# Kernel optimization log

Hardware: AMD Instinct MI355X
Metric: run time of the kernel (lower is better)

## Reference

```python
import jax, jax.numpy as jnp
import numpy as np

LN_EPS = 1e-5
BN_EPS = 1e-5
ALPHA = 0.1

def _layer_norm(x):
    # F.layer_norm over last dim, no affine
    mu = jnp.mean(x, axis=-1, keepdims=True)
    var = jnp.var(x, axis=-1, keepdims=True)
    return (x - mu) * jax.lax.rsqrt(var + LN_EPS)

def setup_inputs() -> dict:
    key = jax.random.key(0)
    ks = jax.random.split(key, 12)
    N, Nh, D, Dq = 8192, 8192, 64, 64
    s = 1.0 / np.sqrt(D)
    inp = {
        "X": jax.random.normal(ks[0], (N, D), jnp.float32),
        "H": jax.random.normal(ks[1], (Nh, D), jnp.float32),
        "M": jax.random.uniform(ks[2], (N, Nh), jnp.float32),
        # Linear params (torch nn.Linear: y = x @ W.T + b), uniform init scale
        "Qw": jax.random.uniform(ks[3], (Dq, D), jnp.float32, -s, s),
        "Qb": jax.random.uniform(ks[4], (Dq,), jnp.float32, -s, s),
        "Kw": jax.random.uniform(ks[5], (Dq, D), jnp.float32, -s, s),
        "Kb": jax.random.uniform(ks[6], (Dq,), jnp.float32, -s, s),
        "Vw": jax.random.uniform(ks[7], (64, D), jnp.float32, -s, s),
        "Vb": jax.random.uniform(ks[8], (64,), jnp.float32, -s, s),
        # BatchNorm1d(64) eval-mode params
        "bn_gamma": jnp.ones((64,), jnp.float32),
        "bn_beta": jnp.zeros((64,), jnp.float32),
        "bn_mean": 0.1 * jax.random.normal(ks[9], (64,), jnp.float32),
        "bn_var": jax.random.uniform(ks[10], (64,), jnp.float32, 0.5, 1.5),
    }
    return inp

def reference(X, H, M, Qw, Qb, Kw, Kb, Vw, Vb, bn_gamma, bn_beta, bn_mean, bn_var):
    # K/Q branches: Linear + LayerNorm
    K = _layer_norm(H @ Kw.T + Kb)            # [Nh, Dq]
    Q = _layer_norm(X @ Qw.T + Qb)            # [N, Dq]
    # V branch: Linear + BatchNorm1d (eval mode; dropout is identity in eval)
    V = (H @ Vw.T + Vb - bn_mean) * jax.lax.rsqrt(bn_var + BN_EPS) * bn_gamma + bn_beta  # [Nh, 64]
    # Masked attention, softmax over dim=0 (columns)
    A = (Q @ K.T) * 0.125                     # [N, Nh]
    A = jax.nn.softmax(M * A, axis=0)
    # globel=True branch
    return ALPHA * (A @ V) + M @ H            # [N, 64]
```

## Files before the change

kernel.cpp:

```cpp
#include <hip/hip_runtime.h>
#include <hip/hip_bf16.h>
#include <math.h>

#define NN 8192
#define QSCALE (0.125f * 1.44269504088896f)
#define OSZ (8192*64)
#define NSL 16

typedef __attribute__((ext_vector_type(8))) short short8;
typedef __attribute__((ext_vector_type(16))) float f32x16;
typedef __attribute__((ext_vector_type(4))) float f32x4;

union W4 { unsigned u[4]; short8 v; };

__device__ inline unsigned short f2bf(float x) {
  union { float f; unsigned u; } t; t.f = x;
  unsigned r = t.u + 0x7fffu + ((t.u >> 16) & 1u);
  return (unsigned short)(r >> 16);
}
__device__ inline unsigned cvtpk(float lo, float hi) {
  unsigned r;
  asm("v_cvt_pk_bf16_f32 %0, %1, %2" : "=v"(r) : "v"(lo), "v"(hi));
  return r;
}
__device__ inline float fexp2(float x) {
  float r;
  asm("v_exp_f32 %0, %1" : "=v"(r) : "v"(x));
  return r;
}
__device__ inline void gload16(const float* g, float* l) {
  __builtin_amdgcn_global_load_lds(
      (const __attribute__((address_space(1))) void*)g,
      (__attribute__((address_space(3))) void*)l, 16, 0, 0);
}

__global__ __launch_bounds__(256) void qkv_kernel(
    const float* __restrict__ X, const float* __restrict__ H,
    const float* __restrict__ Qw, const float* __restrict__ Qb,
    const float* __restrict__ Kw, const float* __restrict__ Kb,
    const float* __restrict__ Vw, const float* __restrict__ Vb,
    const float* __restrict__ bng, const float* __restrict__ bnb,
    const float* __restrict__ bnm, const float* __restrict__ bnv,
    unsigned short* __restrict__ QP, unsigned short* __restrict__ KP,
    unsigned short* __restrict__ VP, unsigned short* __restrict__ HP)
{
  int wid = (blockIdx.x * blockDim.x + threadIdx.x) >> 6;
  int d = threadIdx.x & 63;
  float4 w[16];

  for (int fq = 0; fq < 16; fq++) w[fq] = *(const float4*)(Qw + d*64 + fq*4);
  for (int rr = 0; rr < 4; rr++) {
    int r = wid*4 + rr;
    float a = Qb[d];
    for (int fq = 0; fq < 16; fq++) {
      float4 xv = *(const float4*)(X + r*64 + fq*4);
      a += w[fq].x*xv.x + w[fq].y*xv.y + w[fq].z*xv.z + w[fq].w*xv.w;
    }
    float s = a;
    for (int off = 32; off; off >>= 1) s += __shfl_xor(s, off);
    float mean = s * (1.f/64.f);
    float c = a - mean;
    float s2 = c*c;
    for (int off = 32; off; off >>= 1) s2 += __shfl_xor(s2, off);
    float q = c * rsqrtf(s2*(1.f/64.f) + 1e-5f);
    QP[(d>>3)*65536 + r*8 + (d&7)] = f2bf(q * QSCALE);
  }
  for (int fq = 0; fq < 16; fq++) w[fq] = *(const float4*)(Kw + d*64 + fq*4);
  for (int rr = 0; rr < 4; rr++) {
    int r = wid*4 + rr;
    float a = Kb[d];
    for (int fq = 0; fq < 16; fq++) {
      float4 hv = *(const float4*)(H + r*64 + fq*4);
      a += w[fq].x*hv.x + w[fq].y*hv.y + w[fq].z*hv.z + w[fq].w*hv.w;
    }
    float s = a;
    for (int off = 32; off; off >>= 1) s += __shfl_xor(s, off);
    float mean = s * (1.f/64.f);
    float c = a - mean;
    float s2 = c*c;
    for (int off = 32; off; off >>= 1) s2 += __shfl_xor(s2, off);
    float k = c * rsqrtf(s2*(1.f/64.f) + 1e-5f);
    KP[(d>>3)*65536 + r*8 + (d&7)] = f2bf(k);
  }
  for (int fq = 0; fq < 16; fq++) w[fq] = *(const float4*)(Vw + d*64 + fq*4);
  float bscale = rsqrtf(bnv[d] + 1e-5f) * bng[d];
  for (int rr = 0; rr < 4; rr++) {
    int r = wid*4 + rr;
    float a = Vb[d];
    for (int fq = 0; fq < 16; fq++) {
      float4 hv = *(const float4*)(H + r*64 + fq*4);
      a += w[fq].x*hv.x + w[fq].y*hv.y + w[fq].z*hv.z + w[fq].w*hv.w;
    }
    float v = (a - bnm[d]) * bscale + bnb[d];
    VP[(r>>3)*512 + d*8 + (r&7)] = f2bf(v);
    HP[(r>>3)*512 + d*8 + (r&7)] = f2bf(H[r*64 + d]);
  }
}

__global__ __launch_bounds__(256) void pass1_kernel(
    const float* __restrict__ M, const unsigned short* __restrict__ QP,
    const unsigned short* __restrict__ KP, float* __restrict__ pd)
{
  int tid = threadIdx.x;
  int wj = (blockIdx.x * blockDim.x + tid) >> 6;
  int lane = tid & 63;
  int l31 = lane & 31, h = lane >> 5;
  int jb = wj & 255, slice = wj >> 8;
  int j = jb*32 + l31;

  short8 kb[4];
  for (int m = 0; m < 4; m++)
    kb[m] = *(const short8*)(KP + (2*m + h)*65536 + j*8);

  float Mv[16];
  {
    int i0 = slice*8*32;
#pragma unroll
    for (int r = 0; r < 16; r++) {
      int ir = (r&3) + 8*(r>>2) + 4*h;
      Mv[r] = M[(size_t)(i0 + ir)*NN + j];
    }
  }

  float d0 = 0.f, d1 = 0.f, d2 = 0.f, d3 = 0.f;
  for (int t = 0; t < 8; t++) {
    int i0 = (slice*8 + t) * 32;
    float Mn[16];
    if (t < 7) {
      int i1 = i0 + 32;
#pragma unroll
      for (int r = 0; r < 16; r++) {
        int ir = (r&3) + 8*(r>>2) + 4*h;
        Mn[r] = M[(size_t)(i1 + ir)*NN + j];
      }
    }

    f32x16 acc;
    for (int r = 0; r < 16; r++) acc[r] = 0.f;
    for (int m = 0; m < 4; m++) {
      short8 qa = *(const short8*)(QP + (2*m + h)*65536 + (size_t)(i0 + l31)*8);
      acc = __builtin_amdgcn_mfma_f32_32x32x16_bf16(qa, kb[m], acc, 0, 0, 0);
    }

    d0 += fexp2(acc[0]*Mv[0]) + fexp2(acc[4]*Mv[4]) + fexp2(acc[8]*Mv[8])   + fexp2(acc[12]*Mv[12]);
    d1 += fexp2(acc[1]*Mv[1]) + fexp2(acc[5]*Mv[5]) + fexp2(acc[9]*Mv[9])   + fexp2(acc[13]*Mv[13]);
    d2 += fexp2(acc[2]*Mv[2]) + fexp2(acc[6]*Mv[6]) + fexp2(acc[10]*Mv[10]) + fexp2(acc[14]*Mv[14]);
    d3 += fexp2(acc[3]*Mv[3]) + fexp2(acc[7]*Mv[7]) + fexp2(acc[11]*Mv[11]) + fexp2(acc[15]*Mv[15]);

    if (t < 7) {
#pragma unroll
      for (int r = 0; r < 16; r++) Mv[r] = Mn[r];
    }
  }
  float drun = (d0 + d1) + (d2 + d3);
  drun += __shfl_xor(drun, 32);
  if (lane < 32) pd[(size_t)slice*NN + j] = drun;
}

__global__ __launch_bounds__(256) void cv_kernel(
    const float* __restrict__ pd, const unsigned short* __restrict__ VP,
    unsigned short* __restrict__ VP2)
{
  __shared__ float cls[256];
  int tid = threadIdx.x;
  int j = blockIdx.x * 256 + tid;
  float Dv = 0.f;
  for (int s = 0; s < 32; s++) Dv += pd[(size_t)s*NN + j];
  cls[tid] = 0.1f / Dv;
  __syncthreads();

  int base = blockIdx.x * 2048;
#pragma unroll
  for (int k = 0; k < 8; k++) {
    int idx = base + k*256 + tid;
    int lj8 = (k*256 + tid) >> 6;
    const unsigned short* src = VP + (size_t)idx*8;
    unsigned short sv[8];
    *(short8*)sv = *(const short8*)src;
    float f[8];
#pragma unroll
    for (int e = 0; e < 8; e++)
      f[e] = __uint_as_float(((unsigned)sv[e]) << 16) * cls[lj8*8 + e];
    W4 o;
    o.u[0] = cvtpk(f[0], f[1]); o.u[1] = cvtpk(f[2], f[3]);
    o.u[2] = cvtpk(f[4], f[5]); o.u[3] = cvtpk(f[6], f[7]);
    *(short8*)(VP2 + (size_t)idx*8) = o.v;
  }
}

__global__ __launch_bounds__(256) void pass2_kernel(
    const float* __restrict__ M, const unsigned short* __restrict__ QP,
    const unsigned short* __restrict__ KP, const unsigned short* __restrict__ VP2,
    const unsigned short* __restrict__ HP, float* __restrict__ opart)
{
  __shared__ __align__(16) float tile[3][64*32];

  int iblk = blockIdx.x >> 4, slice = blockIdx.x & 15;
  int i0 = iblk * 64;
  int tid = threadIdx.x;
  int lane = tid & 63, wv = tid >> 6;
  int l31 = lane & 31, h = lane >> 5;
  int iq = wv & 1, dh = wv >> 1;
  int i_g = i0 + iq*32 + l31;
  int row = iq*32 + l31;
  int r7 = row & 7;

  short8 qb[4];
#pragma unroll
  for (int m = 0; m < 4; m++)
    qb[m] = *(const short8*)(QP + (2*m + h)*65536 + (size_t)i_g*8);

  int rsub = lane >> 3;
  int gdst = lane & 7;
  int c0base = slice*512;

#pragma unroll
  for (int t0 = 0; t0 < 2; t0++) {
    int c0 = c0base + t0*32;
#pragma unroll
    for (int k = 0; k < 2; k++) {
      int rloc = wv*16 + k*8 + rsub;
      int gs = gdst ^ (rloc & 7);
      gload16(M + (size_t)(i0 + rloc)*NN + c0 + gs*4,
              &tile[t0][(wv*16 + k*8)*32]);
    }
  }
  asm volatile("s_waitcnt vmcnt(2)" ::: "memory");
  __builtin_amdgcn_s_barrier();
  __builtin_amdgcn_sched_barrier(0);

  f32x16 oaccV, oaccH;
  for (int r = 0; r < 16; r++) { oaccV[r] = 0.f; oaccH[r] = 0.f; }

  for (int tm = 0; tm < 16; tm++) {
    int jt = slice*512 + tm*32;
    const float* mb = tile[tm % 3];

    short8 kb[4];
#pragma unroll
    for (int m = 0; m < 4; m++)
      kb[m] = *(const short8*)(KP + (2*m + h)*65536 + (size_t)(jt + l31)*8);
    int j8 = jt >> 3;
    const unsigned short* vbase = VP2 + (size_t)j8*512 + (dh*32 + l31)*8;
    const unsigned short* hbase = HP  + (size_t)j8*512 + (dh*32 + l31)*8;
    short8 vb1 = *(const short8*)(vbase + h*512);
    short8 vb2 = *(const short8*)(vbase + (2 + h)*512);
    short8 hb1 = *(const short8*)(hbase + h*512);
    short8 hb2 = *(const short8*)(hbase + (2 + h)*512);

    if (tm < 14) {
      int c0 = c0base + (tm+2)*32;
      float* dst = tile[(tm+2) % 3];
#pragma unroll
      for (int k = 0; k < 2; k++) {
        int rloc = wv*16 + k*8 + rsub;
        int gs = gdst ^ (rloc & 7);
        gload16(M + (size_t)(i0 + rloc)*NN + c0 + gs*4,
                &dst[(wv*16 + k*8)*32]);
      }
    }

    f32x4 mv[4];
#pragma unroll
    for (int q = 0; q < 4; q++) {
      int gr = 2*q + h;
      mv[q] = *(const f32x4*)&mb[row*32 + ((gr ^ r7) << 2)];
    }

    f32x16 saccA, saccB;
    for (int r = 0; r < 16; r++) { saccA[r] = 0.f; saccB[r] = 0.f; }
    saccA = __builtin_amdgcn_mfma_f32_32x32x16_bf16(kb[0], qb[0], saccA, 0, 0, 0);
    saccB = __builtin_amdgcn_mfma_f32_32x32x16_bf16(kb[2], qb[2], saccB, 0, 0, 0);
    saccA = __builtin_amdgcn_mfma_f32_32x32x16_bf16(kb[1], qb[1], saccA, 0, 0, 0);
    saccB = __builtin_amdgcn_mfma_f32_32x32x16_bf16(kb[3], qb[3], saccB, 0, 0, 0);

    float p[16];
#pragma unroll
    for (int q = 0; q < 4; q++) {
      p[4*q+0] = fexp2((saccA[4*q+0] + saccB[4*q+0]) * mv[q][0]);
      p[4*q+1] = fexp2((saccA[4*q+1] + saccB[4*q+1]) * mv[q][1]);
      p[4*q+2] = fexp2((saccA[4*q+2] + saccB[4*q+2]) * mv[q][2]);
      p[4*q+3] = fexp2((saccA[4*q+3] + saccB[4*q+3]) * mv[q][3]);
    }
    unsigned pu[8], mw[8];
#pragma unroll
    for (int k = 0; k < 8; k++) pu[k] = cvtpk(p[2*k], p[2*k+1]);
#pragma unroll
    for (int q = 0; q < 4; q++) {
      mw[2*q]   = cvtpk(mv[q][0], mv[q][1]);
      mw[2*q+1] = cvtpk(mv[q][2], mv[q][3]);
    }

    asm volatile("v_permlane32_swap_b32 %0, %1" : "+v"(pu[0]), "+v"(pu[2]));
    asm volatile("v_permlane32_swap_b32 %0, %1" : "+v"(pu[1]), "+v"(pu[3]));
    asm volatile("v_permlane32_swap_b32 %0, %1" : "+v"(pu[4]), "+v"(pu[6]));
    asm volatile("v_permlane32_swap_b32 %0, %1" : "+v"(pu[5]), "+v"(pu[7]));
    asm volatile("v_permlane32_swap_b32 %0, %1" : "+v"(mw[0]), "+v"(mw[2]));
    asm volatile("v_permlane32_swap_b32 %0, %1" : "+v"(mw[1]), "+v"(mw[3]));
    asm volatile("v_permlane32_swap_b32 %0, %1" : "+v"(mw[4]), "+v"(mw[6]));
    asm volatile("v_permlane32_swap_b32 %0, %1" : "+v"(mw[5]), "+v"(mw[7]));

    W4 PA0, PA1, MA0, MA1;
    PA0.u[0] = pu[0]; PA0.u[1] = pu[1]; PA0.u[2] = pu[2]; PA0.u[3] = pu[3];
    PA1.u[0] = pu[4]; PA1.u[1] = pu[5]; PA1.u[2] = pu[6]; PA1.u[3] = pu[7];
    MA0.u[0] = mw[0]; MA0.u[1] = mw[1]; MA0.u[2] = mw[2]; MA0.u[3] = mw[3];
    MA1.u[0] = mw[4]; MA1.u[1] = mw[5]; MA1.u[2] = mw[6]; MA1.u[3] = mw[7];

    oaccV = __builtin_amdgcn_mfma_f32_32x32x16_bf16(PA0.v, vb1, oaccV, 0, 0, 0);
    oaccH = __builtin_amdgcn_mfma_f32_32x32x16_bf16(MA0.v, hb1, oaccH, 0, 0, 0);
    oaccV = __builtin_amdgcn_mfma_f32_32x32x16_bf16(PA1.v, vb2, oaccV, 0, 0, 0);
    oaccH = __builtin_amdgcn_mfma_f32_32x32x16_bf16(MA1.v, hb2, oaccH, 0, 0, 0);

    if (tm < 14) {
      asm volatile("s_waitcnt vmcnt(2)" ::: "memory");
    } else {
      asm volatile("s_waitcnt vmcnt(0)" ::: "memory");
    }
    __builtin_amdgcn_s_barrier();
    __builtin_amdgcn_sched_barrier(0);
  }

  float* obase = opart + (size_t)slice*OSZ;
#pragma unroll
  for (int r = 0; r < 16; r++) {
    int orow = i0 + iq*32 + (r&3) + 8*(r>>2) + 4*h;
    int ocol = dh*32 + l31;
    obase[(size_t)orow*64 + ocol] = oaccV[r] + oaccH[r];
  }
}

__global__ __launch_bounds__(256) void reduce_kernel(
    const float* __restrict__ opart, float* __restrict__ out)
{
  int e4 = blockIdx.x * blockDim.x + threadIdx.x;
  const float4* p = (const float4*)opart;
  float4 a = p[e4];
#pragma unroll
  for (int s = 1; s < NSL; s++) {
    float4 b = p[(size_t)s*(OSZ/4) + e4];
    a.x += b.x; a.y += b.y; a.z += b.z; a.w += b.w;
  }
  ((float4*)out)[e4] = a;
}

extern "C" void kernel_launch(void* const* d_in, const int* in_sizes, int n_in,
                              void* d_out, int out_size, void* d_ws, size_t ws_size,
                              hipStream_t stream) {
  const float* X   = (const float*)d_in[0];
  const float* H   = (const float*)d_in[1];
  const float* M   = (const float*)d_in[2];
  const float* Qw  = (const float*)d_in[3];
  const float* Qb  = (const float*)d_in[4];
  const float* Kw  = (const float*)d_in[5];
  const float* Kb  = (const float*)d_in[6];
  const float* Vw  = (const float*)d_in[7];
  const float* Vb  = (const float*)d_in[8];
  const float* bng = (const float*)d_in[9];
  const float* bnb = (const float*)d_in[10];
  const float* bnm = (const float*)d_in[11];
  const float* bnv = (const float*)d_in[12];
  float* out = (float*)d_out;

  char* ws = (char*)d_ws;
  const size_t MB = 1024*1024;
  unsigned short* QP  = (unsigned short*)(ws);
  unsigned short* KP  = (unsigned short*)(ws + 1*MB);
  unsigned short* VP  = (unsigned short*)(ws + 2*MB);
  unsigned short* HP  = (unsigned short*)(ws + 3*MB);
  unsigned short* VP2 = (unsigned short*)(ws + 4*MB);
  float* pd           = (float*)(ws + 5*MB);
  float* opart        = (float*)(ws + 7*MB);

  qkv_kernel<<<512, 256, 0, stream>>>(X, H, Qw, Qb, Kw, Kb, Vw, Vb,
                                      bng, bnb, bnm, bnv, QP, KP, VP, HP);
  pass1_kernel<<<2048, 256, 0, stream>>>(M, QP, KP, pd);
  cv_kernel<<<32, 256, 0, stream>>>(pd, VP, VP2);
  pass2_kernel<<<2048, 256, 0, stream>>>(M, QP, KP, VP2, HP, opart);
  reduce_kernel<<<512, 256, 0, stream>>>(opart, out);
}
```

Baseline: 206.3 us.

## Give each pass2 wave a distinct row tile and cover all 64 output columns

The pass2 kernel now tiles 128 rows per block, with each of the four waves owning 32 distinct rows. Previously pairs of waves duplicated the same QK^T score MFMAs and exp work for different output column halves. Each wave now computes the scores once and accumulates both 32-column output halves, which removes redundant score and exp computation and halves the grid. The cost is fewer blocks, fewer waves for latency hiding, and more accumulator registers. The M-tile pipeline also shrinks from triple to double buffering, with a plain __syncthreads replacing the tuned vmcnt waits.

```diff
diff --git a/kernel.cpp b/kernel.cpp
--- a/kernel.cpp
+++ b/kernel.cpp
@@ -193,17 +193,16 @@
     const unsigned short* __restrict__ KP, const unsigned short* __restrict__ VP2,
     const unsigned short* __restrict__ HP, float* __restrict__ opart)
 {
-  __shared__ __align__(16) float tile[3][64*32];
+  __shared__ __align__(16) float tile[2][128*32];
 
   int iblk = blockIdx.x >> 4, slice = blockIdx.x & 15;
-  int i0 = iblk * 64;
+  int i0 = iblk * 128;
   int tid = threadIdx.x;
   int lane = tid & 63, wv = tid >> 6;
   int l31 = lane & 31, h = lane >> 5;
-  int iq = wv & 1, dh = wv >> 1;
-  int i_g = i0 + iq*32 + l31;
-  int row = iq*32 + l31;
-  int r7 = row & 7;
+  int irow = wv*32 + l31;
+  int i_g = i0 + irow;
+  int r7 = irow & 7;
 
   short8 qb[4];
 #pragma unroll
@@ -215,72 +214,58 @@
   int c0base = slice*512;
 
 #pragma unroll
-  for (int t0 = 0; t0 < 2; t0++) {
-    int c0 = c0base + t0*32;
-#pragma unroll
-    for (int k = 0; k < 2; k++) {
-      int rloc = wv*16 + k*8 + rsub;
-      int gs = gdst ^ (rloc & 7);
-      gload16(M + (size_t)(i0 + rloc)*NN + c0 + gs*4,
-              &tile[t0][(wv*16 + k*8)*32]);
-    }
-  }
-  asm volatile("s_waitcnt vmcnt(2)" ::: "memory");
-  __builtin_amdgcn_s_barrier();
-  __builtin_amdgcn_sched_barrier(0);
-
-  f32x16 oaccV, oaccH;
-  for (int r = 0; r < 16; r++) { oaccV[r] = 0.f; oaccH[r] = 0.f; }
+  for (int k = 0; k < 4; k++) {
+    int rloc = wv*32 + k*8 + rsub;
+    int gs = gdst ^ (rloc & 7);
+    gload16(M + (size_t)(i0 + rloc)*NN + c0base + gs*4,
+            &tile[0][(wv*32 + k*8)*32]);
+  }
+  __syncthreads();
+
+  f32x16 oaccA, oaccB;
+  for (int r = 0; r < 16; r++) { oaccA[r] = 0.f; oaccB[r] = 0.f; }
 
   for (int tm = 0; tm < 16; tm++) {
     int jt = slice*512 + tm*32;
-    const float* mb = tile[tm % 3];
+
+    if (tm < 15) {
+      int c0 = c0base + (tm+1)*32;
+      float* dst = tile[(tm+1) & 1];
+#pragma unroll
+      for (int k = 0; k < 4; k++) {
+        int rloc = wv*32 + k*8 + rsub;
+        int gs = gdst ^ (rloc & 7);
+        gload16(M + (size_t)(i0 + rloc)*NN + c0 + gs*4,
+                &dst[(wv*32 + k*8)*32]);
+      }
+    }
+    const float* mb = tile[tm & 1];
 
     short8 kb[4];
 #pragma unroll
     for (int m = 0; m < 4; m++)
       kb[m] = *(const short8*)(KP + (2*m + h)*65536 + (size_t)(jt + l31)*8);
-    int j8 = jt >> 3;
-    const unsigned short* vbase = VP2 + (size_t)j8*512 + (dh*32 + l31)*8;
-    const unsigned short* hbase = HP  + (size_t)j8*512 + (dh*32 + l31)*8;
-    short8 vb1 = *(const short8*)(vbase + h*512);
-    short8 vb2 = *(const short8*)(vbase + (2 + h)*512);
-    short8 hb1 = *(const short8*)(hbase + h*512);
-    short8 hb2 = *(const short8*)(hbase + (2 + h)*512);
-
-    if (tm < 14) {
-      int c0 = c0base + (tm+2)*32;
-      float* dst = tile[(tm+2) % 3];
-#pragma unroll
-      for (int k = 0; k < 2; k++) {
-        int rloc = wv*16 + k*8 + rsub;
-        int gs = gdst ^ (rloc & 7);
-        gload16(M + (size_t)(i0 + rloc)*NN + c0 + gs*4,
-                &dst[(wv*16 + k*8)*32]);
-      }
-    }
 
     f32x4 mv[4];
 #pragma unroll
     for (int q = 0; q < 4; q++) {
       int gr = 2*q + h;
-      mv[q] = *(const f32x4*)&mb[row*32 + ((gr ^ r7) << 2)];
-    }
-
-    f32x16 saccA, saccB;
-    for (int r = 0; r < 16; r++) { saccA[r] = 0.f; saccB[r] = 0.f; }
-    saccA = __builtin_amdgcn_mfma_f32_32x32x16_bf16(kb[0], qb[0], saccA, 0, 0, 0);
-    saccB = __builtin_amdgcn_mfma_f32_32x32x16_bf16(kb[2], qb[2], saccB, 0, 0, 0);
-    saccA = __builtin_amdgcn_mfma_f32_32x32x16_bf16(kb[1], qb[1], saccA, 0, 0, 0);
-    saccB = __builtin_amdgcn_mfma_f32_32x32x16_bf16(kb[3], qb[3], saccB, 0, 0, 0);
+      mv[q] = *(const f32x4*)&mb[irow*32 + ((gr ^ r7) << 2)];
+    }
+
+    f32x16 sacc;
+    for (int r = 0; r < 16; r++) sacc[r] = 0.f;
+#pragma unroll
+    for (int m = 0; m < 4; m++)
+      sacc = __builtin_amdgcn_mfma_f32_32x32x16_bf16(kb[m], qb[m], sacc, 0, 0, 0);
 
     float p[16];
 #pragma unroll
     for (int q = 0; q < 4; q++) {
-      p[4*q+0] = fexp2((saccA[4*q+0] + saccB[4*q+0]) * mv[q][0]);
-      p[4*q+1] = fexp2((saccA[4*q+1] + saccB[4*q+1]) * mv[q][1]);
-      p[4*q+2] = fexp2((saccA[4*q+2] + saccB[4*q+2]) * mv[q][2]);
-      p[4*q+3] = fexp2((saccA[4*q+3] + saccB[4*q+3]) * mv[q][3]);
+      p[4*q+0] = fexp2(sacc[4*q+0] * mv[q][0]);
+      p[4*q+1] = fexp2(sacc[4*q+1] * mv[q][1]);
+      p[4*q+2] = fexp2(sacc[4*q+2] * mv[q][2]);
+      p[4*q+3] = fexp2(sacc[4*q+3] * mv[q][3]);
     }
     unsigned pu[8], mw[8];
 #pragma unroll
@@ -306,26 +291,39 @@
     MA0.u[0] = mw[0]; MA0.u[1] = mw[1]; MA0.u[2] = mw[2]; MA0.u[3] = mw[3];
     MA1.u[0] = mw[4]; MA1.u[1] = mw[5]; MA1.u[2] = mw[6]; MA1.u[3] = mw[7];
 
-    oaccV = __builtin_amdgcn_mfma_f32_32x32x16_bf16(PA0.v, vb1, oaccV, 0, 0, 0);
-    oaccH = __builtin_amdgcn_mfma_f32_32x32x16_bf16(MA0.v, hb1, oaccH, 0, 0, 0);
-    oaccV = __builtin_amdgcn_mfma_f32_32x32x16_bf16(PA1.v, vb2, oaccV, 0, 0, 0);
-    oaccH = __builtin_amdgcn_mfma_f32_32x32x16_bf16(MA1.v, hb2, oaccH, 0, 0, 0);
-
-    if (tm < 14) {
-      asm volatile("s_waitcnt vmcnt(2)" ::: "memory");
-    } else {
-      asm volatile("s_waitcnt vmcnt(0)" ::: "memory");
-    }
-    __builtin_amdgcn_s_barrier();
-    __builtin_amdgcn_sched_barrier(0);
+    int j8 = jt >> 3;
+    const unsigned short* vb_ = VP2 + (size_t)j8*512 + l31*8;
+    const unsigned short* hb_ = HP  + (size_t)j8*512 + l31*8;
+    {
+      short8 vA1 = *(const short8*)(vb_ + h*512);
+      short8 vA2 = *(const short8*)(vb_ + (2 + h)*512);
+      short8 hA1 = *(const short8*)(hb_ + h*512);
+      short8 hA2 = *(const short8*)(hb_ + (2 + h)*512);
+      oaccA = __builtin_amdgcn_mfma_f32_32x32x16_bf16(PA0.v, vA1, oaccA, 0, 0, 0);
+      oaccA = __builtin_amdgcn_mfma_f32_32x32x16_bf16(PA1.v, vA2, oaccA, 0, 0, 0);
+      oaccA = __builtin_amdgcn_mfma_f32_32x32x16_bf16(MA0.v, hA1, oaccA, 0, 0, 0);
+      oaccA = __builtin_amdgcn_mfma_f32_32x32x16_bf16(MA1.v, hA2, oaccA, 0, 0, 0);
+    }
+    {
+      short8 vB1 = *(const short8*)(vb_ + 256 + h*512);
+      short8 vB2 = *(const short8*)(vb_ + 256 + (2 + h)*512);
+      short8 hB1 = *(const short8*)(hb_ + 256 + h*512);
+      short8 hB2 = *(const short8*)(hb_ + 256 + (2 + h)*512);
+      oaccB = __builtin_amdgcn_mfma_f32_32x32x16_bf16(PA0.v, vB1, oaccB, 0, 0, 0);
+      oaccB = __builtin_amdgcn_mfma_f32_32x32x16_bf16(PA1.v, vB2, oaccB, 0, 0, 0);
+      oaccB = __builtin_amdgcn_mfma_f32_32x32x16_bf16(MA0.v, hB1, oaccB, 0, 0, 0);
+      oaccB = __builtin_amdgcn_mfma_f32_32x32x16_bf16(MA1.v, hB2, oaccB, 0, 0, 0);
+    }
+
+    __syncthreads();
   }
 
   float* obase = opart + (size_t)slice*OSZ;
 #pragma unroll
   for (int r = 0; r < 16; r++) {
-    int orow = i0 + iq*32 + (r&3) + 8*(r>>2) + 4*h;
-    int ocol = dh*32 + l31;
-    obase[(size_t)orow*64 + ocol] = oaccV[r] + oaccH[r];
+    int orow = i0 + wv*32 + (r&3) + 8*(r>>2) + 4*h;
+    obase[(size_t)orow*64 + l31]      = oaccA[r];
+    obase[(size_t)orow*64 + 32 + l31] = oaccB[r];
   }
 }
 
@@ -375,6 +373,6 @@
                                       bng, bnb, bnm, bnv, QP, KP, VP, HP);
   pass1_kernel<<<2048, 256, 0, stream>>>(M, QP, KP, pd);
   cv_kernel<<<32, 256, 0, stream>>>(pd, VP, VP2);
-  pass2_kernel<<<2048, 256, 0, stream>>>(M, QP, KP, VP2, HP, opart);
+  pass2_kernel<<<1024, 256, 0, stream>>>(M, QP, KP, VP2, HP, opart);
   reduce_kernel<<<512, 256, 0, stream>>>(opart, out);
 }
```

After: 171.0 us. 17.1% less time.
